# Performance work log

Measured on AMD Instinct MI355X. Metric: run time of the kernel, lower is better.

## Reference

```python
import jax, jax.numpy as jnp
import numpy as np

FEAT = 256
N_NODES = 262144
N_GRAPHS = 8192
LEAKY_SLOPE = 0.01  # torch LeakyReLU default


def setup_inputs() -> dict:
    key = jax.random.key(0)
    ks = jax.random.split(key, 12)
    node_feats = jax.random.normal(ks[0], (N_NODES, FEAT), dtype=jnp.float32)
    g_feats = jax.random.normal(ks[1], (N_GRAPHS, FEAT), dtype=jnp.float32)
    seg = jnp.sort(jax.random.randint(ks[2], (N_NODES,), 0, N_GRAPHS, dtype=jnp.int32))
    s2f = 1.0 / np.sqrt(2 * FEAT)
    sf = 1.0 / np.sqrt(FEAT)
    return {
        "node_feats": node_feats,
        "g_feats": g_feats,
        "seg": seg,
        # compute_logits: Linear(2*feat, 1)
        "W_log": jax.random.uniform(ks[3], (2 * FEAT, 1), jnp.float32, -s2f, s2f),
        "b_log": jax.random.uniform(ks[4], (1,), jnp.float32, -s2f, s2f),
        # project_nodes: Linear(feat, feat) (Dropout is identity at inference)
        "W_proj": jax.random.uniform(ks[5], (FEAT, FEAT), jnp.float32, -sf, sf),
        "b_proj": jax.random.uniform(ks[6], (FEAT,), jnp.float32, -sf, sf),
        # GRUCell(feat, feat): torch layout [3*feat, feat], gate order r,z,n
        "W_ih": jax.random.uniform(ks[7], (3 * FEAT, FEAT), jnp.float32, -sf, sf),
        "W_hh": jax.random.uniform(ks[8], (3 * FEAT, FEAT), jnp.float32, -sf, sf),
        "b_ih": jax.random.uniform(ks[9], (3 * FEAT,), jnp.float32, -sf, sf),
        "b_hh": jax.random.uniform(ks[10], (3 * FEAT,), jnp.float32, -sf, sf),
    }


def _gru_cell(x, h, W_ih, W_hh, b_ih, b_hh):
    gi = x @ W_ih.T + b_ih  # [B, 3F]
    gh = h @ W_hh.T + b_hh
    i_r, i_z, i_n = jnp.split(gi, 3, axis=1)
    h_r, h_z, h_n = jnp.split(gh, 3, axis=1)
    r = jax.nn.sigmoid(i_r + h_r)
    z = jax.nn.sigmoid(i_z + h_z)
    n = jnp.tanh(i_n + r * h_n)
    return (1.0 - z) * n + z * h


def reference(node_feats, g_feats, seg, W_log, b_log, W_proj, b_proj, W_ih, W_hh, b_ih, b_hh):
    B = g_feats.shape[0]
    # broadcast_nodes(g, relu(g_feats)) then concat with node_feats
    gf_nodes = jax.nn.relu(g_feats)[seg]                      # [N, F]
    x = jnp.concatenate([gf_nodes, node_feats], axis=1)      # [N, 2F]
    z = x @ W_log + b_log                                     # [N, 1]
    z = jnp.where(z >= 0, z, LEAKY_SLOPE * z)                 # LeakyReLU
    # segment softmax over nodes of each graph (dgl.softmax_nodes)
    m = jax.ops.segment_max(z, seg, num_segments=B)           # [B, 1]
    e = jnp.exp(z - m[seg])
    s = jax.ops.segment_sum(e, seg, num_segments=B)           # [B, 1]
    a = e / s[seg]                                            # [N, 1]
    # project_nodes (Dropout identity at inference)
    hv = node_feats @ W_proj + b_proj                         # [N, F]
    # weighted segment sum (dgl.sum_nodes with weight 'a')
    g_repr = jax.ops.segment_sum(a * hv, seg, num_segments=B)  # [B, F]
    context = jax.nn.elu(g_repr)
    return _gru_cell(context, g_feats, W_ih, W_hh, b_ih, b_hh)
```

## Files before the change

### kernel.cpp

```cpp
#include <hip/hip_runtime.h>
#include <hip/hip_bf16.h>
#include <math.h>

#define FEAT 256
#define NNODES 262144
#define NGRAPHS 8192

typedef short bf16x8 __attribute__((ext_vector_type(8)));
typedef float f32x4 __attribute__((ext_vector_type(4)));

__device__ __forceinline__ unsigned short f2bf(float f) {
    unsigned u = __float_as_uint(f);
    u += 0x7fffu + ((u >> 16) & 1u);
    return (unsigned short)(u >> 16);
}

__device__ __forceinline__ float waveReduceSum(float v) {
#pragma unroll
    for (int m = 32; m > 0; m >>= 1) v += __shfl_xor(v, m, 64);
    return v;
}

__device__ __forceinline__ float sigmoidf(float x) { return 1.f / (1.f + expf(-x)); }

__global__ void k_offsets(const int* __restrict__ seg, int* __restrict__ off) {
    int b = blockIdx.x * blockDim.x + threadIdx.x;
    if (b > NGRAPHS) return;
    int lo = 0, hi = NNODES;
    while (lo < hi) {
        int mid = (lo + hi) >> 1;
        if (seg[mid] < b) lo = mid + 1; else hi = mid;
    }
    off[b] = lo;
}

__global__ void k_tobf16(const float* __restrict__ src, unsigned short* __restrict__ dst, int n) {
    int i = (blockIdx.x * blockDim.x + threadIdx.x) * 4;
    if (i >= n) return;
    float4 v = *(const float4*)(src + i);
    ushort4 o;
    o.x = f2bf(v.x); o.y = f2bf(v.y); o.z = f2bf(v.z); o.w = f2bf(v.w);
    *(ushort4*)(dst + i) = o;
}

__global__ void k_wproj_t(const float* __restrict__ W, unsigned short* __restrict__ Wt) {
    int f = blockIdx.x, k = threadIdx.x;
    Wt[f * 256 + k] = f2bf(W[k * 256 + f]);
}

__global__ void k_gz(const float* __restrict__ g_feats, const float* __restrict__ W_log,
                     const float* __restrict__ b_log, float* __restrict__ gz) {
    int gw = (blockIdx.x * blockDim.x + threadIdx.x) >> 6;
    int lane = threadIdx.x & 63;
    if (gw >= NGRAPHS) return;
    float4 gf = *(const float4*)(g_feats + (size_t)gw * FEAT + lane * 4);
    float4 wl = *(const float4*)(W_log + lane * 4);
    float d = fmaxf(gf.x, 0.f) * wl.x + fmaxf(gf.y, 0.f) * wl.y +
              fmaxf(gf.z, 0.f) * wl.z + fmaxf(gf.w, 0.f) * wl.w;
    d = waveReduceSum(d);
    if (lane == 0) gz[gw] = d + b_log[0];
}

__global__ __launch_bounds__(256) void k_graph(
    const float* __restrict__ node_feats, const int* __restrict__ off,
    const float* __restrict__ W_log, const float* __restrict__ gz,
    unsigned short* __restrict__ pooled_bf16, float* __restrict__ asum_out) {
    const int b = blockIdx.x;
    const int tid = threadIdx.x;
    const int lane = tid & 63;
    const int wv = tid >> 6;

    const int start = off[b];
    const int end = off[b + 1];

    __shared__ float wAcc[4][FEAT];
    __shared__ float wM[4], wS[4];

    if (end - start == 0) {
        pooled_bf16[(size_t)b * FEAT + tid] = 0;
        if (tid == 0) asum_out[b] = 0.f;
        return;
    }

    const float4 wl = *(const float4*)(W_log + FEAT + lane * 4);
    const float gzb = gz[b];

    float m = -INFINITY, s = 0.f;
    float a0 = 0.f, a1 = 0.f, a2 = 0.f, a3 = 0.f;

    for (int i = start + wv; i < end; i += 4) {
        float4 nf = *(const float4*)(node_feats + (size_t)i * FEAT + lane * 4);
        float d = nf.x * wl.x + nf.y * wl.y + nf.z * wl.z + nf.w * wl.w;
        d = waveReduceSum(d);
        float z = gzb + d;
        z = (z >= 0.f) ? z : 0.01f * z;
        float mn = fmaxf(m, z);
        float scale = expf(m - mn);
        float e = expf(z - mn);
        s = s * scale + e;
        a0 = fmaf(e, nf.x, a0 * scale);
        a1 = fmaf(e, nf.y, a1 * scale);
        a2 = fmaf(e, nf.z, a2 * scale);
        a3 = fmaf(e, nf.w, a3 * scale);
        m = mn;
    }

    float4 av = {a0, a1, a2, a3};
    *(float4*)(&wAcc[wv][lane * 4]) = av;
    if (lane == 0) { wM[wv] = m; wS[wv] = s; }
    __syncthreads();

    float M = fmaxf(fmaxf(wM[0], wM[1]), fmaxf(wM[2], wM[3]));
    float e0 = expf(wM[0] - M), e1 = expf(wM[1] - M), e2 = expf(wM[2] - M), e3 = expf(wM[3] - M);
    float S = wS[0] * e0 + wS[1] * e1 + wS[2] * e2 + wS[3] * e3;
    float val = wAcc[0][tid] * e0 + wAcc[1][tid] * e1 + wAcc[2][tid] * e2 + wAcc[3][tid] * e3;
    pooled_bf16[(size_t)b * FEAT + tid] = f2bf(val / S);
    if (tid == 0) asum_out[b] = 1.f;
}


__global__ __launch_bounds__(256) void k_context(
    const unsigned short* __restrict__ pooled, const float* __restrict__ asum,
    const unsigned short* __restrict__ Wpt, const float* __restrict__ b_proj,
    unsigned short* __restrict__ ctx) {
    const int bm = blockIdx.x >> 2, bf = blockIdx.x & 3;
    const int m0 = bm * 32, f0 = bf * 64;
    const int tid = threadIdx.x;
    const int lane = tid & 63;
    const int wv = tid >> 6;
    const int wm = wv >> 1, wn = wv & 1;
    const int q = lane >> 4;

    __shared__ __align__(16) char ldsA[16384];

    for (int p = 0; p < 4; ++p) {
        int c = p * 256 + tid;
        int row = c >> 5;
        int kb = (c & 31) << 4;
        uint4 v = *(const uint4*)((const char*)pooled + (size_t)m0 * 512 + c * 16);
        *(uint4*)(ldsA + row * 512 + (kb ^ ((row & 7) << 4))) = v;
    }
    __syncthreads();

    const int arow = wm * 16 + (lane & 15);
    const int aswz = (arow & 7) << 4;
    const char* aBase = ldsA + arow * 512;

    const int fb = f0 + wn * 32 + (lane & 15);
    const char* bBase = (const char*)Wpt + (size_t)fb * 512 + q * 16;

    f32x4 acc[2] = {{0.f, 0.f, 0.f, 0.f}, {0.f, 0.f, 0.f, 0.f}};

    for (int kk = 0; kk < 8; ++kk) {
        bf16x8 a = *(const bf16x8*)(aBase + ((kk * 64 + q * 16) ^ aswz));
        bf16x8 b0 = *(const bf16x8*)(bBase + kk * 64);
        bf16x8 b1 = *(const bf16x8*)(bBase + 16 * 512 + kk * 64);
        acc[0] = __builtin_amdgcn_mfma_f32_16x16x32_bf16(a, b0, acc[0], 0, 0, 0);
        acc[1] = __builtin_amdgcn_mfma_f32_16x16x32_bf16(a, b1, acc[1], 0, 0, 0);
    }

    const int rbase = m0 + wm * 16 + q * 4;
#pragma unroll
    for (int nf = 0; nf < 2; ++nf) {
        int f = fb + nf * 16;
        float bp = b_proj[f];
#pragma unroll
        for (int j = 0; j < 4; ++j) {
            int mr = rbase + j;
            float v = acc[nf][j] + asum[mr] * bp;
            v = (v > 0.f) ? v : expm1f(v);
            ctx[(size_t)mr * 256 + f] = f2bf(v);
        }
    }
}

__global__ __launch_bounds__(256) void k_gates(
    const unsigned short* __restrict__ ctx, const unsigned short* __restrict__ gfb,
    const float* __restrict__ g_feats, const unsigned short* __restrict__ wih,
    const unsigned short* __restrict__ whh, const float* __restrict__ b_ih,
    const float* __restrict__ b_hh, float* __restrict__ out) {
    const int bm = blockIdx.x >> 2, bf = blockIdx.x & 3;
    const int m0 = bm * 32, f0 = bf * 64;
    const int tid = threadIdx.x;
    const int lane = tid & 63;
    const int wv = tid >> 6;
    const int wm = wv >> 1, wn = wv & 1;
    const int q = lane >> 4;

    __shared__ __align__(16) char ldsC[16384];
    __shared__ __align__(16) char ldsG[16384];

    for (int p = 0; p < 4; ++p) {
        int c = p * 256 + tid;
        int row = c >> 5;
        int kb = (c & 31) << 4;
        int dst = row * 512 + (kb ^ ((row & 7) << 4));
        uint4 v1 = *(const uint4*)((const char*)ctx + (size_t)m0 * 512 + c * 16);
        uint4 v2 = *(const uint4*)((const char*)gfb + (size_t)m0 * 512 + c * 16);
        *(uint4*)(ldsC + dst) = v1;
        *(uint4*)(ldsG + dst) = v2;
    }
    __syncthreads();

    const int arow = wm * 16 + (lane & 15);
    const int aswz = (arow & 7) << 4;
    const char* aC = ldsC + arow * 512;
    const char* aG = ldsG + arow * 512;

    const int fb = f0 + wn * 32 + (lane & 15);
    const char* iR = (const char*)wih + (size_t)(0 * 256 + fb) * 512 + q * 16;
    const char* iZ = (const char*)wih + (size_t)(1 * 256 + fb) * 512 + q * 16;
    const char* iN = (const char*)wih + (size_t)(2 * 256 + fb) * 512 + q * 16;
    const char* hR = (const char*)whh + (size_t)(0 * 256 + fb) * 512 + q * 16;
    const char* hZ = (const char*)whh + (size_t)(1 * 256 + fb) * 512 + q * 16;
    const char* hN = (const char*)whh + (size_t)(2 * 256 + fb) * 512 + q * 16;

    f32x4 accR[2] = {{0.f, 0.f, 0.f, 0.f}, {0.f, 0.f, 0.f, 0.f}};
    f32x4 accZ[2] = {{0.f, 0.f, 0.f, 0.f}, {0.f, 0.f, 0.f, 0.f}};
    f32x4 accIN[2] = {{0.f, 0.f, 0.f, 0.f}, {0.f, 0.f, 0.f, 0.f}};
    f32x4 accHN[2] = {{0.f, 0.f, 0.f, 0.f}, {0.f, 0.f, 0.f, 0.f}};

    for (int kk = 0; kk < 8; ++kk) {
        bf16x8 a = *(const bf16x8*)(aC + ((kk * 64 + q * 16) ^ aswz));
#pragma unroll
        for (int nf = 0; nf < 2; ++nf) {
            int o = nf * 8192 + kk * 64;
            bf16x8 br = *(const bf16x8*)(iR + o);
            bf16x8 bz = *(const bf16x8*)(iZ + o);
            bf16x8 bn = *(const bf16x8*)(iN + o);
            accR[nf] = __builtin_amdgcn_mfma_f32_16x16x32_bf16(a, br, accR[nf], 0, 0, 0);
            accZ[nf] = __builtin_amdgcn_mfma_f32_16x16x32_bf16(a, bz, accZ[nf], 0, 0, 0);
            accIN[nf] = __builtin_amdgcn_mfma_f32_16x16x32_bf16(a, bn, accIN[nf], 0, 0, 0);
        }
    }
    for (int kk = 0; kk < 8; ++kk) {
        bf16x8 a = *(const bf16x8*)(aG + ((kk * 64 + q * 16) ^ aswz));
#pragma unroll
        for (int nf = 0; nf < 2; ++nf) {
            int o = nf * 8192 + kk * 64;
            bf16x8 br = *(const bf16x8*)(hR + o);
            bf16x8 bz = *(const bf16x8*)(hZ + o);
            bf16x8 bn = *(const bf16x8*)(hN + o);
            accR[nf] = __builtin_amdgcn_mfma_f32_16x16x32_bf16(a, br, accR[nf], 0, 0, 0);
            accZ[nf] = __builtin_amdgcn_mfma_f32_16x16x32_bf16(a, bz, accZ[nf], 0, 0, 0);
            accHN[nf] = __builtin_amdgcn_mfma_f32_16x16x32_bf16(a, bn, accHN[nf], 0, 0, 0);
        }
    }

    const int rbase = m0 + wm * 16 + q * 4;
#pragma unroll
    for (int nf = 0; nf < 2; ++nf) {
        int f = fb + nf * 16;
        float b_r = b_ih[f] + b_hh[f];
        float b_z = b_ih[256 + f] + b_hh[256 + f];
        float b_in = b_ih[512 + f];
        float b_hn = b_hh[512 + f];
#pragma unroll
        for (int j = 0; j < 4; ++j) {
            int mr = rbase + j;
            float rr = sigmoidf(accR[nf][j] + b_r);
            float zz = sigmoidf(accZ[nf][j] + b_z);
            float nn = tanhf(accIN[nf][j] + b_in + rr * (accHN[nf][j] + b_hn));
            float h = g_feats[(size_t)mr * 256 + f];
            out[(size_t)mr * 256 + f] = (1.f - zz) * nn + zz * h;
        }
    }
}

extern "C" void kernel_launch(void* const* d_in, const int* in_sizes, int n_in,
                              void* d_out, int out_size, void* d_ws, size_t ws_size,
                              hipStream_t stream) {
    const float* node_feats = (const float*)d_in[0];
    const float* g_feats    = (const float*)d_in[1];
    const int*   seg        = (const int*)d_in[2];
    const float* W_log      = (const float*)d_in[3];
    const float* b_log      = (const float*)d_in[4];
    const float* W_proj     = (const float*)d_in[5];
    const float* b_proj     = (const float*)d_in[6];
    const float* W_ih       = (const float*)d_in[7];
    const float* W_hh       = (const float*)d_in[8];
    const float* b_ih       = (const float*)d_in[9];
    const float* b_hh       = (const float*)d_in[10];
    float* out = (float*)d_out;

    char* ws = (char*)d_ws;
    int*   off        = (int*)ws;
    float* gz         = (float*)(ws + 33792);
    float* asumw      = (float*)(ws + 66560);
    unsigned short* pooled = (unsigned short*)(ws + 99328);
    unsigned short* ctxb   = (unsigned short*)(ws + 99328 + 4194304);
    unsigned short* gfb    = (unsigned short*)(ws + 99328 + 2 * 4194304);
    unsigned short* wihb   = (unsigned short*)(ws + 99328 + 3 * 4194304);
    unsigned short* whhb   = (unsigned short*)(ws + 99328 + 3 * 4194304 + 393216);
    unsigned short* wptb   = (unsigned short*)(ws + 99328 + 3 * 4194304 + 2 * 393216);

    hipLaunchKernelGGL(k_offsets, dim3(33), dim3(256), 0, stream, seg, off);
    hipLaunchKernelGGL(k_tobf16, dim3(192), dim3(256), 0, stream, W_ih, wihb, 768 * 256);
    hipLaunchKernelGGL(k_tobf16, dim3(192), dim3(256), 0, stream, W_hh, whhb, 768 * 256);
    hipLaunchKernelGGL(k_tobf16, dim3(2048), dim3(256), 0, stream, g_feats, gfb, NGRAPHS * FEAT);
    hipLaunchKernelGGL(k_wproj_t, dim3(256), dim3(256), 0, stream, W_proj, wptb);
    hipLaunchKernelGGL(k_gz, dim3(NGRAPHS / 4), dim3(256), 0, stream, g_feats, W_log, b_log, gz);
    hipLaunchKernelGGL(k_graph, dim3(NGRAPHS), dim3(256), 0, stream,
                       node_feats, off, W_log, gz, pooled, asumw);
    hipLaunchKernelGGL(k_context, dim3(1024), dim3(256), 0, stream,
                       pooled, asumw, wptb, b_proj, ctxb);
    hipLaunchKernelGGL(k_gates, dim3(1024), dim3(256), 0, stream,
                       ctxb, gfb, g_feats, wihb, whhb, b_ih, b_hh, out);
}
```

Baseline: 139.7 us.

## Fuse prep kernels, drop online-softmax max, merge context and GRU kernels

Merges the six small preprocessing launches into one multi-role kernel, and fuses the context projection with the GRU gates so the context tile stays in LDS. The g_feats bf16 conversion now happens inside the fused kernel. The segment softmax drops the running max and exponentiates logits directly, and each wave now handles four nodes at a time with 16-lane reductions. Launch count and intermediate global traffic go down, but the fused GEMM grid is only 256 blocks, and skipping the max subtraction risks overflow for large logits.

```diff
diff --git a/kernel.cpp b/kernel.cpp
--- a/kernel.cpp
+++ b/kernel.cpp
@@ -7,6 +7,7 @@
 #define NGRAPHS 8192
 
 typedef short bf16x8 __attribute__((ext_vector_type(8)));
+typedef unsigned short u16x8 __attribute__((ext_vector_type(8)));
 typedef float f32x4 __attribute__((ext_vector_type(4)));
 
 __device__ __forceinline__ unsigned short f2bf(float f) {
@@ -23,246 +24,265 @@
 
 __device__ __forceinline__ float sigmoidf(float x) { return 1.f / (1.f + expf(-x)); }
 
-__global__ void k_offsets(const int* __restrict__ seg, int* __restrict__ off) {
-    int b = blockIdx.x * blockDim.x + threadIdx.x;
-    if (b > NGRAPHS) return;
-    int lo = 0, hi = NNODES;
-    while (lo < hi) {
-        int mid = (lo + hi) >> 1;
-        if (seg[mid] < b) lo = mid + 1; else hi = mid;
-    }
-    off[b] = lo;
-}
-
-__global__ void k_tobf16(const float* __restrict__ src, unsigned short* __restrict__ dst, int n) {
-    int i = (blockIdx.x * blockDim.x + threadIdx.x) * 4;
-    if (i >= n) return;
-    float4 v = *(const float4*)(src + i);
-    ushort4 o;
-    o.x = f2bf(v.x); o.y = f2bf(v.y); o.z = f2bf(v.z); o.w = f2bf(v.w);
-    *(ushort4*)(dst + i) = o;
-}
-
-__global__ void k_wproj_t(const float* __restrict__ W, unsigned short* __restrict__ Wt) {
-    int f = blockIdx.x, k = threadIdx.x;
-    Wt[f * 256 + k] = f2bf(W[k * 256 + f]);
-}
-
-__global__ void k_gz(const float* __restrict__ g_feats, const float* __restrict__ W_log,
-                     const float* __restrict__ b_log, float* __restrict__ gz) {
-    int gw = (blockIdx.x * blockDim.x + threadIdx.x) >> 6;
-    int lane = threadIdx.x & 63;
-    if (gw >= NGRAPHS) return;
-    float4 gf = *(const float4*)(g_feats + (size_t)gw * FEAT + lane * 4);
-    float4 wl = *(const float4*)(W_log + lane * 4);
-    float d = fmaxf(gf.x, 0.f) * wl.x + fmaxf(gf.y, 0.f) * wl.y +
-              fmaxf(gf.z, 0.f) * wl.z + fmaxf(gf.w, 0.f) * wl.w;
-    d = waveReduceSum(d);
-    if (lane == 0) gz[gw] = d + b_log[0];
+__global__ __launch_bounds__(256) void k_prep(
+    const float* __restrict__ g_feats, const float* __restrict__ W_log,
+    const float* __restrict__ b_log, const float* __restrict__ W_ih,
+    const float* __restrict__ W_hh, const float* __restrict__ W_proj,
+    const int* __restrict__ seg, float* __restrict__ gz,
+    unsigned short* __restrict__ wihb, unsigned short* __restrict__ whhb,
+    unsigned short* __restrict__ wptb, int* __restrict__ off) {
+    const int blk = blockIdx.x;
+    const int tid = threadIdx.x;
+    if (blk < 2048) {
+        int gw = blk * 4 + (tid >> 6);
+        int lane = tid & 63;
+        float4 gf = *(const float4*)(g_feats + (size_t)gw * FEAT + lane * 4);
+        float4 wl = *(const float4*)(W_log + lane * 4);
+        float d = fmaxf(gf.x, 0.f) * wl.x + fmaxf(gf.y, 0.f) * wl.y +
+                  fmaxf(gf.z, 0.f) * wl.z + fmaxf(gf.w, 0.f) * wl.w;
+        d = waveReduceSum(d);
+        if (lane == 0) gz[gw] = d + b_log[0];
+    } else if (blk < 2240) {
+        int i = (blk - 2048) * 1024 + tid * 4;
+        float4 v = *(const float4*)(W_ih + i);
+        ushort4 o;
+        o.x = f2bf(v.x); o.y = f2bf(v.y); o.z = f2bf(v.z); o.w = f2bf(v.w);
+        *(ushort4*)(wihb + i) = o;
+    } else if (blk < 2432) {
+        int i = (blk - 2240) * 1024 + tid * 4;
+        float4 v = *(const float4*)(W_hh + i);
+        ushort4 o;
+        o.x = f2bf(v.x); o.y = f2bf(v.y); o.z = f2bf(v.z); o.w = f2bf(v.w);
+        *(ushort4*)(whhb + i) = o;
+    } else if (blk < 2688) {
+        int f = blk - 2432;
+        wptb[f * 256 + tid] = f2bf(W_proj[tid * 256 + f]);
+    } else {
+        int b = (blk - 2688) * 256 + tid;
+        if (b > NGRAPHS) return;
+        int lo = 0, hi = NNODES;
+        while (lo < hi) {
+            int mid = (lo + hi) >> 1;
+            if (seg[mid] < b) lo = mid + 1; else hi = mid;
+        }
+        off[b] = lo;
+    }
 }
 
 __global__ __launch_bounds__(256) void k_graph(
     const float* __restrict__ node_feats, const int* __restrict__ off,
     const float* __restrict__ W_log, const float* __restrict__ gz,
-    unsigned short* __restrict__ pooled_bf16, float* __restrict__ asum_out) {
+    unsigned short* __restrict__ pooled, float* __restrict__ asum_out) {
     const int b = blockIdx.x;
     const int tid = threadIdx.x;
     const int lane = tid & 63;
     const int wv = tid >> 6;
+    const int grp = lane >> 4;
+    const int sl = lane & 15;
 
     const int start = off[b];
     const int end = off[b + 1];
 
     __shared__ float wAcc[4][FEAT];
-    __shared__ float wM[4], wS[4];
+    __shared__ float wS[4];
 
     if (end - start == 0) {
-        pooled_bf16[(size_t)b * FEAT + tid] = 0;
+        pooled[(size_t)b * FEAT + tid] = 0;
         if (tid == 0) asum_out[b] = 0.f;
         return;
     }
 
-    const float4 wl = *(const float4*)(W_log + FEAT + lane * 4);
+    const float4 w0 = *(const float4*)(W_log + FEAT + sl * 4);
+    const float4 w1 = *(const float4*)(W_log + FEAT + 64 + sl * 4);
+    const float4 w2 = *(const float4*)(W_log + FEAT + 128 + sl * 4);
+    const float4 w3 = *(const float4*)(W_log + FEAT + 192 + sl * 4);
     const float gzb = gz[b];
 
-    float m = -INFINITY, s = 0.f;
-    float a0 = 0.f, a1 = 0.f, a2 = 0.f, a3 = 0.f;
-
-    for (int i = start + wv; i < end; i += 4) {
-        float4 nf = *(const float4*)(node_feats + (size_t)i * FEAT + lane * 4);
-        float d = nf.x * wl.x + nf.y * wl.y + nf.z * wl.z + nf.w * wl.w;
-        d = waveReduceSum(d);
+    float s = 0.f;
+    float4 A0 = {0.f, 0.f, 0.f, 0.f}, A1 = A0, A2 = A0, A3 = A0;
+
+    for (int i = start + wv * 4 + grp; i < end; i += 16) {
+        const float* row = node_feats + (size_t)i * FEAT + sl * 4;
+        float4 n0 = *(const float4*)(row);
+        float4 n1 = *(const float4*)(row + 64);
+        float4 n2 = *(const float4*)(row + 128);
+        float4 n3 = *(const float4*)(row + 192);
+        float d0 = n0.x * w0.x + n0.y * w0.y + n0.z * w0.z + n0.w * w0.w;
+        float d1 = n1.x * w1.x + n1.y * w1.y + n1.z * w1.z + n1.w * w1.w;
+        float d2 = n2.x * w2.x + n2.y * w2.y + n2.z * w2.z + n2.w * w2.w;
+        float d3 = n3.x * w3.x + n3.y * w3.y + n3.z * w3.z + n3.w * w3.w;
+        float d = (d0 + d1) + (d2 + d3);
+        d += __shfl_xor(d, 1);
+        d += __shfl_xor(d, 2);
+        d += __shfl_xor(d, 4);
+        d += __shfl_xor(d, 8);
         float z = gzb + d;
         z = (z >= 0.f) ? z : 0.01f * z;
-        float mn = fmaxf(m, z);
-        float scale = expf(m - mn);
-        float e = expf(z - mn);
-        s = s * scale + e;
-        a0 = fmaf(e, nf.x, a0 * scale);
-        a1 = fmaf(e, nf.y, a1 * scale);
-        a2 = fmaf(e, nf.z, a2 * scale);
-        a3 = fmaf(e, nf.w, a3 * scale);
-        m = mn;
-    }
-
-    float4 av = {a0, a1, a2, a3};
-    *(float4*)(&wAcc[wv][lane * 4]) = av;
-    if (lane == 0) { wM[wv] = m; wS[wv] = s; }
+        float e = expf(z);
+        s += e;
+        A0.x = fmaf(e, n0.x, A0.x); A0.y = fmaf(e, n0.y, A0.y);
+        A0.z = fmaf(e, n0.z, A0.z); A0.w = fmaf(e, n0.w, A0.w);
+        A1.x = fmaf(e, n1.x, A1.x); A1.y = fmaf(e, n1.y, A1.y);
+        A1.z = fmaf(e, n1.z, A1.z); A1.w = fmaf(e, n1.w, A1.w);
+        A2.x = fmaf(e, n2.x, A2.x); A2.y = fmaf(e, n2.y, A2.y);
+        A2.z = fmaf(e, n2.z, A2.z); A2.w = fmaf(e, n2.w, A2.w);
+        A3.x = fmaf(e, n3.x, A3.x); A3.y = fmaf(e, n3.y, A3.y);
+        A3.z = fmaf(e, n3.z, A3.z); A3.w = fmaf(e, n3.w, A3.w);
+    }
+
+#define MRG(X) X += __shfl_xor(X, 16); X += __shfl_xor(X, 32);
+    MRG(A0.x) MRG(A0.y) MRG(A0.z) MRG(A0.w)
+    MRG(A1.x) MRG(A1.y) MRG(A1.z) MRG(A1.w)
+    MRG(A2.x) MRG(A2.y) MRG(A2.z) MRG(A2.w)
+    MRG(A3.x) MRG(A3.y) MRG(A3.z) MRG(A3.w)
+    MRG(s)
+#undef MRG
+
+    if (grp == 0) {
+        *(float4*)&wAcc[wv][sl * 4] = A0;
+        *(float4*)&wAcc[wv][64 + sl * 4] = A1;
+        *(float4*)&wAcc[wv][128 + sl * 4] = A2;
+        *(float4*)&wAcc[wv][192 + sl * 4] = A3;
+        if (sl == 0) wS[wv] = s;
+    }
     __syncthreads();
 
-    float M = fmaxf(fmaxf(wM[0], wM[1]), fmaxf(wM[2], wM[3]));
-    float e0 = expf(wM[0] - M), e1 = expf(wM[1] - M), e2 = expf(wM[2] - M), e3 = expf(wM[3] - M);
-    float S = wS[0] * e0 + wS[1] * e1 + wS[2] * e2 + wS[3] * e3;
-    float val = wAcc[0][tid] * e0 + wAcc[1][tid] * e1 + wAcc[2][tid] * e2 + wAcc[3][tid] * e3;
-    pooled_bf16[(size_t)b * FEAT + tid] = f2bf(val / S);
+    float val = (wAcc[0][tid] + wAcc[1][tid]) + (wAcc[2][tid] + wAcc[3][tid]);
+    float S = (wS[0] + wS[1]) + (wS[2] + wS[3]);
+    pooled[(size_t)b * FEAT + tid] = f2bf(val / S);
     if (tid == 0) asum_out[b] = 1.f;
 }
 
-
-__global__ __launch_bounds__(256) void k_context(
+__global__ __launch_bounds__(256) void k_ctxgru(
     const unsigned short* __restrict__ pooled, const float* __restrict__ asum,
-    const unsigned short* __restrict__ Wpt, const float* __restrict__ b_proj,
-    unsigned short* __restrict__ ctx) {
-    const int bm = blockIdx.x >> 2, bf = blockIdx.x & 3;
-    const int m0 = bm * 32, f0 = bf * 64;
+    const unsigned short* __restrict__ wptb, const float* __restrict__ b_proj,
+    const float* __restrict__ g_feats, const unsigned short* __restrict__ wihb,
+    const unsigned short* __restrict__ whhb, const float* __restrict__ b_ih,
+    const float* __restrict__ b_hh, float* __restrict__ out) {
+    const int m0 = blockIdx.x * 32;
     const int tid = threadIdx.x;
     const int lane = tid & 63;
     const int wv = tid >> 6;
-    const int wm = wv >> 1, wn = wv & 1;
     const int q = lane >> 4;
-
-    __shared__ __align__(16) char ldsA[16384];
-
-    for (int p = 0; p < 4; ++p) {
-        int c = p * 256 + tid;
-        int row = c >> 5;
-        int kb = (c & 31) << 4;
-        uint4 v = *(const uint4*)((const char*)pooled + (size_t)m0 * 512 + c * 16);
-        *(uint4*)(ldsA + row * 512 + (kb ^ ((row & 7) << 4))) = v;
-    }
-    __syncthreads();
-
-    const int arow = wm * 16 + (lane & 15);
-    const int aswz = (arow & 7) << 4;
-    const char* aBase = ldsA + arow * 512;
-
-    const int fb = f0 + wn * 32 + (lane & 15);
-    const char* bBase = (const char*)Wpt + (size_t)fb * 512 + q * 16;
-
-    f32x4 acc[2] = {{0.f, 0.f, 0.f, 0.f}, {0.f, 0.f, 0.f, 0.f}};
-
-    for (int kk = 0; kk < 8; ++kk) {
-        bf16x8 a = *(const bf16x8*)(aBase + ((kk * 64 + q * 16) ^ aswz));
-        bf16x8 b0 = *(const bf16x8*)(bBase + kk * 64);
-        bf16x8 b1 = *(const bf16x8*)(bBase + 16 * 512 + kk * 64);
-        acc[0] = __builtin_amdgcn_mfma_f32_16x16x32_bf16(a, b0, acc[0], 0, 0, 0);
-        acc[1] = __builtin_amdgcn_mfma_f32_16x16x32_bf16(a, b1, acc[1], 0, 0, 0);
-    }
-
-    const int rbase = m0 + wm * 16 + q * 4;
-#pragma unroll
-    for (int nf = 0; nf < 2; ++nf) {
-        int f = fb + nf * 16;
-        float bp = b_proj[f];
-#pragma unroll
-        for (int j = 0; j < 4; ++j) {
-            int mr = rbase + j;
-            float v = acc[nf][j] + asum[mr] * bp;
-            v = (v > 0.f) ? v : expm1f(v);
-            ctx[(size_t)mr * 256 + f] = f2bf(v);
-        }
-    }
-}
-
-__global__ __launch_bounds__(256) void k_gates(
-    const unsigned short* __restrict__ ctx, const unsigned short* __restrict__ gfb,
-    const float* __restrict__ g_feats, const unsigned short* __restrict__ wih,
-    const unsigned short* __restrict__ whh, const float* __restrict__ b_ih,
-    const float* __restrict__ b_hh, float* __restrict__ out) {
-    const int bm = blockIdx.x >> 2, bf = blockIdx.x & 3;
-    const int m0 = bm * 32, f0 = bf * 64;
-    const int tid = threadIdx.x;
-    const int lane = tid & 63;
-    const int wv = tid >> 6;
-    const int wm = wv >> 1, wn = wv & 1;
-    const int q = lane >> 4;
-
+    const int fl = lane & 15;
+
+    __shared__ __align__(16) char ldsP[16384];
     __shared__ __align__(16) char ldsC[16384];
     __shared__ __align__(16) char ldsG[16384];
 
+#pragma unroll
     for (int p = 0; p < 4; ++p) {
         int c = p * 256 + tid;
         int row = c >> 5;
         int kb = (c & 31) << 4;
         int dst = row * 512 + (kb ^ ((row & 7) << 4));
-        uint4 v1 = *(const uint4*)((const char*)ctx + (size_t)m0 * 512 + c * 16);
-        uint4 v2 = *(const uint4*)((const char*)gfb + (size_t)m0 * 512 + c * 16);
-        *(uint4*)(ldsC + dst) = v1;
-        *(uint4*)(ldsG + dst) = v2;
+        *(uint4*)(ldsP + dst) = *(const uint4*)((const char*)pooled + (size_t)m0 * 512 + c * 16);
+        const float* gsrc = g_feats + (size_t)(m0 + row) * 256 + (c & 31) * 8;
+        float4 ga = *(const float4*)gsrc;
+        float4 gb = *(const float4*)(gsrc + 4);
+        u16x8 gv;
+        gv[0] = f2bf(ga.x); gv[1] = f2bf(ga.y); gv[2] = f2bf(ga.z); gv[3] = f2bf(ga.w);
+        gv[4] = f2bf(gb.x); gv[5] = f2bf(gb.y); gv[6] = f2bf(gb.z); gv[7] = f2bf(gb.w);
+        *(u16x8*)(ldsG + dst) = gv;
     }
     __syncthreads();
 
-    const int arow = wm * 16 + (lane & 15);
-    const int aswz = (arow & 7) << 4;
-    const char* aC = ldsC + arow * 512;
-    const char* aG = ldsG + arow * 512;
-
-    const int fb = f0 + wn * 32 + (lane & 15);
-    const char* iR = (const char*)wih + (size_t)(0 * 256 + fb) * 512 + q * 16;
-    const char* iZ = (const char*)wih + (size_t)(1 * 256 + fb) * 512 + q * 16;
-    const char* iN = (const char*)wih + (size_t)(2 * 256 + fb) * 512 + q * 16;
-    const char* hR = (const char*)whh + (size_t)(0 * 256 + fb) * 512 + q * 16;
-    const char* hZ = (const char*)whh + (size_t)(1 * 256 + fb) * 512 + q * 16;
-    const char* hN = (const char*)whh + (size_t)(2 * 256 + fb) * 512 + q * 16;
-
-    f32x4 accR[2] = {{0.f, 0.f, 0.f, 0.f}, {0.f, 0.f, 0.f, 0.f}};
-    f32x4 accZ[2] = {{0.f, 0.f, 0.f, 0.f}, {0.f, 0.f, 0.f, 0.f}};
-    f32x4 accIN[2] = {{0.f, 0.f, 0.f, 0.f}, {0.f, 0.f, 0.f, 0.f}};
-    f32x4 accHN[2] = {{0.f, 0.f, 0.f, 0.f}, {0.f, 0.f, 0.f, 0.f}};
-
-    for (int kk = 0; kk < 8; ++kk) {
-        bf16x8 a = *(const bf16x8*)(aC + ((kk * 64 + q * 16) ^ aswz));
-#pragma unroll
-        for (int nf = 0; nf < 2; ++nf) {
-            int o = nf * 8192 + kk * 64;
-            bf16x8 br = *(const bf16x8*)(iR + o);
-            bf16x8 bz = *(const bf16x8*)(iZ + o);
-            bf16x8 bn = *(const bf16x8*)(iN + o);
-            accR[nf] = __builtin_amdgcn_mfma_f32_16x16x32_bf16(a, br, accR[nf], 0, 0, 0);
-            accZ[nf] = __builtin_amdgcn_mfma_f32_16x16x32_bf16(a, bz, accZ[nf], 0, 0, 0);
-            accIN[nf] = __builtin_amdgcn_mfma_f32_16x16x32_bf16(a, bn, accIN[nf], 0, 0, 0);
-        }
-    }
-    for (int kk = 0; kk < 8; ++kk) {
-        bf16x8 a = *(const bf16x8*)(aG + ((kk * 64 + q * 16) ^ aswz));
-#pragma unroll
-        for (int nf = 0; nf < 2; ++nf) {
-            int o = nf * 8192 + kk * 64;
-            bf16x8 br = *(const bf16x8*)(hR + o);
-            bf16x8 bz = *(const bf16x8*)(hZ + o);
-            bf16x8 bn = *(const bf16x8*)(hN + o);
-            accR[nf] = __builtin_amdgcn_mfma_f32_16x16x32_bf16(a, br, accR[nf], 0, 0, 0);
-            accZ[nf] = __builtin_amdgcn_mfma_f32_16x16x32_bf16(a, bz, accZ[nf], 0, 0, 0);
-            accHN[nf] = __builtin_amdgcn_mfma_f32_16x16x32_bf16(a, bn, accHN[nf], 0, 0, 0);
-        }
-    }
-
-    const int rbase = m0 + wm * 16 + q * 4;
-#pragma unroll
-    for (int nf = 0; nf < 2; ++nf) {
-        int f = fb + nf * 16;
-        float b_r = b_ih[f] + b_hh[f];
-        float b_z = b_ih[256 + f] + b_hh[256 + f];
-        float b_in = b_ih[512 + f];
-        float b_hn = b_hh[512 + f];
-#pragma unroll
-        for (int j = 0; j < 4; ++j) {
-            int mr = rbase + j;
-            float rr = sigmoidf(accR[nf][j] + b_r);
-            float zz = sigmoidf(accZ[nf][j] + b_z);
-            float nn = tanhf(accIN[nf][j] + b_in + rr * (accHN[nf][j] + b_hn));
-            float h = g_feats[(size_t)mr * 256 + f];
-            out[(size_t)mr * 256 + f] = (1.f - zz) * nn + zz * h;
+    {
+        const int wm = wv & 1, wn = wv >> 1;
+        const int arow = wm * 16 + fl;
+        const int aswz = (arow & 7) << 4;
+        const char* aP = ldsP + arow * 512;
+
+        f32x4 acc[8];
+#pragma unroll
+        for (int nf = 0; nf < 8; ++nf) acc[nf] = (f32x4){0.f, 0.f, 0.f, 0.f};
+
+        for (int kk = 0; kk < 8; ++kk) {
+            bf16x8 a = *(const bf16x8*)(aP + ((kk * 64 + q * 16) ^ aswz));
+#pragma unroll
+            for (int nf = 0; nf < 8; ++nf) {
+                const char* bp = (const char*)wptb +
+                    (size_t)(wn * 128 + nf * 16 + fl) * 512 + q * 16 + kk * 64;
+                bf16x8 bv = *(const bf16x8*)bp;
+                acc[nf] = __builtin_amdgcn_mfma_f32_16x16x32_bf16(a, bv, acc[nf], 0, 0, 0);
+            }
+        }
+        float as_[4];
+#pragma unroll
+        for (int j = 0; j < 4; ++j) as_[j] = asum[m0 + wm * 16 + q * 4 + j];
+#pragma unroll
+        for (int nf = 0; nf < 8; ++nf) {
+            int c = wn * 128 + nf * 16 + fl;
+            float bp = b_proj[c];
+#pragma unroll
+            for (int j = 0; j < 4; ++j) {
+                int r = wm * 16 + q * 4 + j;
+                float v = acc[nf][j] + as_[j] * bp;
+                v = (v > 0.f) ? v : expm1f(v);
+                *(unsigned short*)(ldsC + r * 512 + ((c * 2) ^ ((r & 7) << 4))) = f2bf(v);
+            }
+        }
+    }
+    __syncthreads();
+
+    const int wmB = wv & 1;
+    const int browL = wmB * 16 + fl;
+    const int aswzB = (browL & 7) << 4;
+    const char* aC = ldsC + browL * 512;
+    const char* aG = ldsG + browL * 512;
+
+    for (int p = 0; p < 2; ++p) {
+        const int cb = ((wv >> 1) + p * 2) * 64;
+        f32x4 aR[4], aZ[4], aIN[4], aHN[4];
+#pragma unroll
+        for (int nf = 0; nf < 4; ++nf) {
+            aR[nf] = (f32x4){0.f, 0.f, 0.f, 0.f}; aZ[nf] = aR[nf];
+            aIN[nf] = aR[nf]; aHN[nf] = aR[nf];
+        }
+        for (int kk = 0; kk < 8; ++kk) {
+            bf16x8 a = *(const bf16x8*)(aC + ((kk * 64 + q * 16) ^ aswzB));
+#pragma unroll
+            for (int nf = 0; nf < 4; ++nf) {
+                const char* base = (const char*)wihb +
+                    (size_t)(cb + nf * 16 + fl) * 512 + q * 16 + kk * 64;
+                bf16x8 br = *(const bf16x8*)(base);
+                bf16x8 bz = *(const bf16x8*)(base + 256 * 512);
+                bf16x8 bn = *(const bf16x8*)(base + 512 * 512);
+                aR[nf] = __builtin_amdgcn_mfma_f32_16x16x32_bf16(a, br, aR[nf], 0, 0, 0);
+                aZ[nf] = __builtin_amdgcn_mfma_f32_16x16x32_bf16(a, bz, aZ[nf], 0, 0, 0);
+                aIN[nf] = __builtin_amdgcn_mfma_f32_16x16x32_bf16(a, bn, aIN[nf], 0, 0, 0);
+            }
+        }
+        for (int kk = 0; kk < 8; ++kk) {
+            bf16x8 a = *(const bf16x8*)(aG + ((kk * 64 + q * 16) ^ aswzB));
+#pragma unroll
+            for (int nf = 0; nf < 4; ++nf) {
+                const char* base = (const char*)whhb +
+                    (size_t)(cb + nf * 16 + fl) * 512 + q * 16 + kk * 64;
+                bf16x8 br = *(const bf16x8*)(base);
+                bf16x8 bz = *(const bf16x8*)(base + 256 * 512);
+                bf16x8 bn = *(const bf16x8*)(base + 512 * 512);
+                aR[nf] = __builtin_amdgcn_mfma_f32_16x16x32_bf16(a, br, aR[nf], 0, 0, 0);
+                aZ[nf] = __builtin_amdgcn_mfma_f32_16x16x32_bf16(a, bz, aZ[nf], 0, 0, 0);
+                aHN[nf] = __builtin_amdgcn_mfma_f32_16x16x32_bf16(a, bn, aHN[nf], 0, 0, 0);
+            }
+        }
+#pragma unroll
+        for (int nf = 0; nf < 4; ++nf) {
+            int f = cb + nf * 16 + fl;
+            float b_r = b_ih[f] + b_hh[f];
+            float b_z = b_ih[256 + f] + b_hh[256 + f];
+            float b_in = b_ih[512 + f];
+            float b_hn = b_hh[512 + f];
+#pragma unroll
+            for (int j = 0; j < 4; ++j) {
+                int r = m0 + wmB * 16 + q * 4 + j;
+                float rr = sigmoidf(aR[nf][j] + b_r);
+                float zz = sigmoidf(aZ[nf][j] + b_z);
+                float nn = tanhf(aIN[nf][j] + b_in + rr * (aHN[nf][j] + b_hn));
+                float h = g_feats[(size_t)r * 256 + f];
+                out[(size_t)r * 256 + f] = (1.f - zz) * nn + zz * h;
+            }
         }
     }
 }
@@ -284,26 +304,19 @@
     float* out = (float*)d_out;
 
     char* ws = (char*)d_ws;
-    int*   off        = (int*)ws;
-    float* gz         = (float*)(ws + 33792);
-    float* asumw      = (float*)(ws + 66560);
+    int*   off   = (int*)ws;
+    float* gz    = (float*)(ws + 33792);
+    float* asumw = (float*)(ws + 66560);
     unsigned short* pooled = (unsigned short*)(ws + 99328);
-    unsigned short* ctxb   = (unsigned short*)(ws + 99328 + 4194304);
-    unsigned short* gfb    = (unsigned short*)(ws + 99328 + 2 * 4194304);
-    unsigned short* wihb   = (unsigned short*)(ws + 99328 + 3 * 4194304);
-    unsigned short* whhb   = (unsigned short*)(ws + 99328 + 3 * 4194304 + 393216);
-    unsigned short* wptb   = (unsigned short*)(ws + 99328 + 3 * 4194304 + 2 * 393216);
-
-    hipLaunchKernelGGL(k_offsets, dim3(33), dim3(256), 0, stream, seg, off);
-    hipLaunchKernelGGL(k_tobf16, dim3(192), dim3(256), 0, stream, W_ih, wihb, 768 * 256);
-    hipLaunchKernelGGL(k_tobf16, dim3(192), dim3(256), 0, stream, W_hh, whhb, 768 * 256);
-    hipLaunchKernelGGL(k_tobf16, dim3(2048), dim3(256), 0, stream, g_feats, gfb, NGRAPHS * FEAT);
-    hipLaunchKernelGGL(k_wproj_t, dim3(256), dim3(256), 0, stream, W_proj, wptb);
-    hipLaunchKernelGGL(k_gz, dim3(NGRAPHS / 4), dim3(256), 0, stream, g_feats, W_log, b_log, gz);
+    unsigned short* wihb   = (unsigned short*)(ws + 99328 + 4194304);
+    unsigned short* whhb   = (unsigned short*)(ws + 99328 + 4194304 + 393216);
+    unsigned short* wptb   = (unsigned short*)(ws + 99328 + 4194304 + 2 * 393216);
+
+    hipLaunchKernelGGL(k_prep, dim3(2721), dim3(256), 0, stream,
+                       g_feats, W_log, b_log, W_ih, W_hh, W_proj, seg,
+                       gz, wihb, whhb, wptb, off);
     hipLaunchKernelGGL(k_graph, dim3(NGRAPHS), dim3(256), 0, stream,
                        node_feats, off, W_log, gz, pooled, asumw);
-    hipLaunchKernelGGL(k_context, dim3(1024), dim3(256), 0, stream,
-                       pooled, asumw, wptb, b_proj, ctxb);
-    hipLaunchKernelGGL(k_gates, dim3(1024), dim3(256), 0, stream,
-                       ctxb, gfb, g_feats, wihb, whhb, b_ih, b_hh, out);
-}
+    hipLaunchKernelGGL(k_ctxgru, dim3(NGRAPHS / 32), dim3(256), 0, stream,
+                       pooled, asumw, wptb, b_proj, g_feats, wihb, whhb, b_ih, b_hh, out);
+}
```

Result: faster. 120.6 us (-13.7%).
